# Optimization experiments

Measured on AMD Instinct MI355X. Metric: run time of the kernel, lower is better.

## Reference

```python
import jax, jax.numpy as jnp
import numpy as np

N = 32768      # total nodes per batched graph
E = 262144     # edges per batched graph (avg in-degree 8)
B = 64         # number of graphs in the batch (for mean_nodes readout)
DIN = 20
H = 512
BN_EPS = 1e-5


def setup_inputs() -> dict:
    key = jax.random.key(0)
    ks = jax.random.split(key, 24)
    p = lambda k, shape: jax.random.normal(k, shape, jnp.float32) * 0.02
    inp = {
        "x1": jax.random.normal(ks[0], (N, DIN), jnp.float32),
        "x2": jax.random.normal(ks[1], (N, DIN), jnp.float32),
        "src1": jax.random.randint(ks[2], (E,), 0, N, jnp.int32),
        "dst1": jax.random.randint(ks[3], (E,), 0, N, jnp.int32),
        "src2": jax.random.randint(ks[4], (E,), 0, N, jnp.int32),
        "dst2": jax.random.randint(ks[5], (E,), 0, N, jnp.int32),
        "gids1": jnp.repeat(jnp.arange(B, dtype=jnp.int32), N // B),
        "gids2": jnp.repeat(jnp.arange(B, dtype=jnp.int32), N // B),
        # shared parameters (applied to both graphs, as in the torch module)
        "W_init": p(ks[6], (DIN, H)), "b_init": jnp.zeros((H,), jnp.float32),
        "W1": p(ks[7], (H, H)), "b1": jnp.zeros((H,), jnp.float32),
        "W2": p(ks[8], (H, H)), "b2": jnp.zeros((H,), jnp.float32),
        "gamma1": jnp.ones((H,), jnp.float32), "beta1": jnp.zeros((H,), jnp.float32),
        "gamma2": jnp.ones((H,), jnp.float32), "beta2": jnp.zeros((H,), jnp.float32),
        "Wfc": p(ks[9], (2 * H, 256)), "bfc": jnp.zeros((256,), jnp.float32),
        "Wfc2": p(ks[10], (256, 1)), "bfc2": jnp.zeros((1,), jnp.float32),
    }
    return inp


def _bn_relu(z, gamma, beta):
    # BatchNorm1d in training mode: biased batch stats over the node axis
    mu = jnp.mean(z, axis=0)
    var = jnp.var(z, axis=0)
    return jax.nn.relu(gamma * (z - mu) * jax.lax.rsqrt(var + BN_EPS) + beta)


def _gin_mean(h, src, dst, W, b):
    # DGL GINConv(apply=Linear, aggregator='mean', eps=0):
    # out = Linear(h + mean_{j in N_in(v)} h_j); isolated nodes get 0 agg.
    msg_sum = jax.ops.segment_sum(h[src], dst, num_segments=N)      # [N,H]
    deg = jax.ops.segment_sum(jnp.ones((src.shape[0],), h.dtype), dst, num_segments=N)
    agg = msg_sum / jnp.maximum(deg, 1.0)[:, None]
    return (h + agg) @ W + b


def _encode(x, src, dst, gids, W_init, b_init, W1, b1, W2, b2,
            gamma1, beta1, gamma2, beta2):
    h0 = x @ W_init + b_init
    h1 = _bn_relu(_gin_mean(h0, src, dst, W1, b1), gamma1, beta1)
    h2 = _bn_relu(_gin_mean(h1, src, dst, W2, b2), gamma2, beta2)
    # dgl.mean_nodes: per-graph mean over nodes
    s = jax.ops.segment_sum(h2, gids, num_segments=B)               # [B,H]
    cnt = jax.ops.segment_sum(jnp.ones((h2.shape[0],), h2.dtype), gids, num_segments=B)
    return s / jnp.maximum(cnt, 1.0)[:, None]


def reference(x1, x2, src1, dst1, src2, dst2, gids1, gids2,
              W_init, b_init, W1, b1, W2, b2,
              gamma1, beta1, gamma2, beta2, Wfc, bfc, Wfc2, bfc2):
    g1_emb = _encode(x1, src1, dst1, gids1, W_init, b_init, W1, b1, W2, b2,
                     gamma1, beta1, gamma2, beta2)
    g2_emb = _encode(x2, src2, dst2, gids2, W_init, b_init, W1, b1, W2, b2,
                     gamma1, beta1, gamma2, beta2)
    x = jnp.concatenate([g1_emb, g2_emb], axis=1)                   # [B,2H]
    x = jax.nn.relu(x @ Wfc + bfc)
    return jax.nn.sigmoid(x @ Wfc2 + bfc2)                          # [B,1]
```

## Files before the change

kernel.cpp:

```cpp
#include <hip/hip_runtime.h>
#include <hip/hip_bf16.h>
#include <cstdint>

#define NN 32768
#define EE 262144
#define MM 65536
#define HH 512
#define BB 64
#define DIN 20
#define BN_EPS 1e-5f

__device__ __forceinline__ float bflo(uint32_t w) { return __builtin_bit_cast(float, w << 16); }
__device__ __forceinline__ float bfhi(uint32_t w) { return __builtin_bit_cast(float, w & 0xffff0000u); }
__device__ __forceinline__ uint32_t f2bf_u(float f) {
  uint32_t u = __builtin_bit_cast(uint32_t, f);
  return (u + 0x7fffu + ((u >> 16) & 1u)) >> 16;
}
__device__ __forceinline__ uint32_t pack2(float lo, float hi) {
  return f2bf_u(lo) | (f2bf_u(hi) << 16);
}

typedef float f32x4 __attribute__((ext_vector_type(4)));
typedef float f32x2 __attribute__((ext_vector_type(2)));

__device__ __forceinline__ void gl2lds16(const void* g, void* l) {
  __builtin_amdgcn_global_load_lds(
      (const __attribute__((address_space(1))) void*)g,
      (__attribute__((address_space(3))) void*)l, 16, 0, 0);
}

__global__ void prep_deg_kernel(const int* __restrict__ dst1, const int* __restrict__ dst2,
                                int* __restrict__ deg_cnt,
                                const float* __restrict__ W2, uint32_t* __restrict__ Wt8,
                                const float* __restrict__ Wi, const float* __restrict__ bi,
                                const float* __restrict__ W1, float* __restrict__ Wf) {
  int bid = blockIdx.x;
  if (bid < 2048) {
    int e = bid * 256 + threadIdx.x;
    int g = e >> 18, le = e & 0x3ffff;
    int d = (g ? dst2 : dst1)[le];
    atomicAdd(&deg_cnt[g * NN + d], 1);
  } else if (bid < 2304) {
    int idx = (bid - 2048) * 256 + threadIdx.x;
    int n = idx >> 7, k4 = idx & 127;
    int k = k4 * 4;
    float w0 = W2[(size_t)k * HH + n];
    float w1 = W2[(size_t)(k + 1) * HH + n];
    float w2v = W2[(size_t)(k + 2) * HH + n];
    float w3 = W2[(size_t)(k + 3) * HH + n];
    uint32_t p = __builtin_amdgcn_cvt_pk_fp8_f32(w0, w1, 0u, false);
    p = __builtin_amdgcn_cvt_pk_fp8_f32(w2v, w3, p, true);
    Wt8[(size_t)n * 128 + k4] = p;
  } else {
    int idx = (bid - 2304) * 256 + threadIdx.x;
    if (idx >= 21 * 512) return;
    int k = idx >> 9, n = idx & 511;
    float s = 0.f;
    if (k < 20) {
      const float* wr = Wi + (size_t)k * HH;
      for (int j = 0; j < HH; j++) s = fmaf(wr[j], W1[(size_t)j * HH + n], s);
    } else {
      for (int j = 0; j < HH; j++) s = fmaf(bi[j], W1[(size_t)j * HH + n], s);
    }
    Wf[idx] = s;
  }
}

__global__ void scan_kernel(const int* __restrict__ deg_cnt, int* __restrict__ offsets,
                            int* __restrict__ cursor) {
  int g = blockIdx.x;
  const int* d = deg_cnt + g * NN;
  int* off = offsets + g * (NN + 1);
  int* cur = cursor + g * NN;
  int t = threadIdx.x;
  int base = t * 32;
  int loc[32]; int s = 0;
#pragma unroll
  for (int i = 0; i < 32; i++) { loc[i] = d[base + i]; s += loc[i]; }
  __shared__ int sm[1024];
  sm[t] = s; __syncthreads();
  for (int ofs = 1; ofs < 1024; ofs <<= 1) {
    int v = sm[t];
    int add = (t >= ofs) ? sm[t - ofs] : 0;
    __syncthreads();
    sm[t] = v + add;
    __syncthreads();
  }
  int run = (t == 0) ? 0 : sm[t - 1];
#pragma unroll
  for (int i = 0; i < 32; i++) { off[base + i] = run; cur[base + i] = run; run += loc[i]; }
  if (t == 1023) off[NN] = run;
}

__global__ void scatter_kernel(const int* __restrict__ src1, const int* __restrict__ dst1,
                               const int* __restrict__ src2, const int* __restrict__ dst2,
                               int* __restrict__ cursor, int* __restrict__ csr) {
  int e = blockIdx.x * 256 + threadIdx.x;
  int g = e >> 18, le = e & 0x3ffff;
  int d = (g ? dst2 : dst1)[le];
  int s = (g ? src2 : src1)[le];
  int pos = atomicAdd(&cursor[g * NN + d], 1);
  csr[g * EE + pos] = s;
}

__global__ __launch_bounds__(512) void z1_kernel(const float* __restrict__ x1,
                          const float* __restrict__ x2,
                          const int* __restrict__ csr, const int* __restrict__ offsets,
                          const float* __restrict__ Wf, const float* __restrict__ b1,
                          uint32_t* __restrict__ z8, float* __restrict__ pstat) {
  __shared__ float xas[128][21];
  __shared__ float sred[512][8];
  int t = threadIdx.x;
  int r0 = blockIdx.x * 128;
  int g = r0 >> 15;
  const float* xg = g ? x2 : x1;
  const int* off = offsets + g * (NN + 1);
  const int* cs = csr + g * EE;

  {
    int row = t >> 2;
    int q = t & 3;
    int n = (r0 + row) & (NN - 1);
    int e0 = off[n], e1 = off[n + 1];
    float4 a4[5] = {};
    for (int e = e0 + q; e < e1; e += 4) {
      const float4* xr = (const float4*)(xg + (size_t)cs[e] * DIN);
#pragma unroll
      for (int k = 0; k < 5; k++) {
        float4 v = xr[k];
        a4[k].x += v.x; a4[k].y += v.y; a4[k].z += v.z; a4[k].w += v.w;
      }
    }
#pragma unroll
    for (int k = 0; k < 5; k++) {
      a4[k].x += __shfl_xor(a4[k].x, 1); a4[k].y += __shfl_xor(a4[k].y, 1);
      a4[k].z += __shfl_xor(a4[k].z, 1); a4[k].w += __shfl_xor(a4[k].w, 1);
      a4[k].x += __shfl_xor(a4[k].x, 2); a4[k].y += __shfl_xor(a4[k].y, 2);
      a4[k].z += __shfl_xor(a4[k].z, 2); a4[k].w += __shfl_xor(a4[k].w, 2);
    }
    if (q == 0) {
      float inv = (e1 > e0) ? 1.f / (float)(e1 - e0) : 0.f;
      const float4* xs = (const float4*)(xg + (size_t)n * DIN);
#pragma unroll
      for (int k = 0; k < 5; k++) {
        float4 v = xs[k];
        xas[row][k * 4 + 0] = fmaf(a4[k].x, inv, v.x);
        xas[row][k * 4 + 1] = fmaf(a4[k].y, inv, v.y);
        xas[row][k * 4 + 2] = fmaf(a4[k].z, inv, v.z);
        xas[row][k * 4 + 3] = fmaf(a4[k].w, inv, v.w);
      }
    }
  }
  __syncthreads();

  int col0 = (t & 127) * 4;
  int rq = t >> 7;

  float w[DIN][4];
#pragma unroll
  for (int k = 0; k < DIN; k++) {
    float4 wv = *(const float4*)(Wf + (size_t)k * HH + col0);
    w[k][0] = wv.x; w[k][1] = wv.y; w[k][2] = wv.z; w[k][3] = wv.w;
  }
  float4 bvv = *(const float4*)(Wf + (size_t)DIN * HH + col0);
  float4 b1v = *(const float4*)(b1 + col0);

  float s4[4] = {0.f, 0.f, 0.f, 0.f}, q4[4] = {0.f, 0.f, 0.f, 0.f};
  for (int rr = 0; rr < 32; rr++) {
    int row = rr * 4 + rq;
    int grow = r0 + row;
    int n = grow & (NN - 1);
    float bf = (off[n + 1] - off[n] > 0) ? 2.f : 1.f;
    float a0 = fmaf(bvv.x, bf, b1v.x), a1 = fmaf(bvv.y, bf, b1v.y);
    float a2 = fmaf(bvv.z, bf, b1v.z), a3 = fmaf(bvv.w, bf, b1v.w);
#pragma unroll
    for (int k = 0; k < DIN; k++) {
      float xv = xas[row][k];
      a0 = fmaf(xv, w[k][0], a0);
      a1 = fmaf(xv, w[k][1], a1);
      a2 = fmaf(xv, w[k][2], a2);
      a3 = fmaf(xv, w[k][3], a3);
    }
    s4[0] += a0; q4[0] = fmaf(a0, a0, q4[0]);
    s4[1] += a1; q4[1] = fmaf(a1, a1, q4[1]);
    s4[2] += a2; q4[2] = fmaf(a2, a2, q4[2]);
    s4[3] += a3; q4[3] = fmaf(a3, a3, q4[3]);
    uint32_t p8 = __builtin_amdgcn_cvt_pk_fp8_f32(a0, a1, 0u, false);
    p8 = __builtin_amdgcn_cvt_pk_fp8_f32(a2, a3, p8, true);
    z8[(size_t)grow * 128 + (col0 >> 2)] = p8;
  }

#pragma unroll
  for (int k = 0; k < 4; k++) { sred[t][k] = s4[k]; sred[t][4 + k] = q4[k]; }
  __syncthreads();
  if (t < 128) {
    float* p = pstat + (size_t)blockIdx.x * 1024 + (size_t)col0 * 2;
#pragma unroll
    for (int k = 0; k < 4; k++) {
      p[k * 2 + 0] = sred[t][k] + sred[t + 128][k] + sred[t + 256][k] + sred[t + 384][k];
      p[k * 2 + 1] = sred[t][4 + k] + sred[t + 128][4 + k] + sred[t + 256][4 + k] + sred[t + 384][4 + k];
    }
  }
}

__global__ void reduce_stats(const float* __restrict__ pstat, const float* __restrict__ gamma,
                             const float* __restrict__ beta, float* __restrict__ scsh) {
  int b = blockIdx.x;
  int g = b >> 4, cg = b & 15;
  int t = threadIdx.x;
  int c = cg * 32 + (t & 31);
  int s = t >> 5;
  const float2* p = (const float2*)pstat + ((size_t)(g * 256 + s * 32)) * 512 + c;
  float sum = 0.f, q = 0.f;
  for (int m = 0; m < 32; m++) { float2 v = p[(size_t)m * 512]; sum += v.x; q += v.y; }
  __shared__ float ls[8][64];
  ls[s][(t & 31) * 2] = sum; ls[s][(t & 31) * 2 + 1] = q;
  __syncthreads();
  if (t < 32) {
    float S = 0.f, Q = 0.f;
#pragma unroll
    for (int k = 0; k < 8; k++) { S += ls[k][t * 2]; Q += ls[k][t * 2 + 1]; }
    int cc = cg * 32 + t;
    float mu = S * (1.f / (float)NN);
    float var = fmaxf(Q * (1.f / (float)NN) - mu * mu, 0.f);
    float sc = gamma[cc] * rsqrtf(var + BN_EPS);
    scsh[g * 1024 + cc * 2] = sc;
    scsh[g * 1024 + cc * 2 + 1] = beta[cc] - mu * sc;
  }
}

__device__ __forceinline__ void bn_acc8_fp8(uint2 v, const float* sc, const float* sh, float* acc) {
  f32x2 f01 = __builtin_amdgcn_cvt_pk_f32_fp8(v.x, false);
  f32x2 f23 = __builtin_amdgcn_cvt_pk_f32_fp8(v.x, true);
  f32x2 f45 = __builtin_amdgcn_cvt_pk_f32_fp8(v.y, false);
  f32x2 f67 = __builtin_amdgcn_cvt_pk_f32_fp8(v.y, true);
  acc[0] += fmaxf(fmaf(f01.x, sc[0], sh[0]), 0.f);
  acc[1] += fmaxf(fmaf(f01.y, sc[1], sh[1]), 0.f);
  acc[2] += fmaxf(fmaf(f23.x, sc[2], sh[2]), 0.f);
  acc[3] += fmaxf(fmaf(f23.y, sc[3], sh[3]), 0.f);
  acc[4] += fmaxf(fmaf(f45.x, sc[4], sh[4]), 0.f);
  acc[5] += fmaxf(fmaf(f45.y, sc[5], sh[5]), 0.f);
  acc[6] += fmaxf(fmaf(f67.x, sc[6], sh[6]), 0.f);
  acc[7] += fmaxf(fmaf(f67.y, sc[7], sh[7]), 0.f);
}

__global__ __launch_bounds__(256) void aggbn_kernel(const uint32_t* __restrict__ z8,
                             uint32_t* __restrict__ u8,
                             const int* __restrict__ csr, const int* __restrict__ offsets,
                             const float* __restrict__ scsh) {
  int wid = (blockIdx.x * 256 + threadIdx.x) >> 6;
  int lane = threadIdx.x & 63;
  int g = wid >> 15, n = wid & (NN - 1);
  const int* off = offsets + g * (NN + 1);
  int e0 = off[n], e1 = off[n + 1];
  const int* cs = csr + g * EE;
  const uint32_t* base8 = z8 + (size_t)g * NN * 128 + lane * 2;

  uint2 hv8 = *(const uint2*)(base8 + (size_t)n * 128);

  const float4* ssp = (const float4*)(scsh + (size_t)g * HH * 2 + lane * 16);
  float4 ss0 = ssp[0], ss1 = ssp[1], ss2 = ssp[2], ss3 = ssp[3];
  float sc[8] = {ss0.x, ss0.z, ss1.x, ss1.z, ss2.x, ss2.z, ss3.x, ss3.z};
  float sh[8] = {ss0.y, ss0.w, ss1.y, ss1.w, ss2.y, ss2.w, ss3.y, ss3.w};
  float acc[8] = {0.f, 0.f, 0.f, 0.f, 0.f, 0.f, 0.f, 0.f};

  int e = e0;
  int rem = e1 - e0;
  int s0 = 0, s1 = 0, s2 = 0, s3 = 0;
  if (rem >= 4) { s0 = cs[e]; s1 = cs[e + 1]; s2 = cs[e + 2]; s3 = cs[e + 3]; }
  while (rem >= 4) {
    uint2 v0 = *(const uint2*)(base8 + (size_t)s0 * 128);
    uint2 v1 = *(const uint2*)(base8 + (size_t)s1 * 128);
    uint2 v2 = *(const uint2*)(base8 + (size_t)s2 * 128);
    uint2 v3 = *(const uint2*)(base8 + (size_t)s3 * 128);
    e += 4; rem -= 4;
    if (rem >= 4) { s0 = cs[e]; s1 = cs[e + 1]; s2 = cs[e + 2]; s3 = cs[e + 3]; }
    bn_acc8_fp8(v0, sc, sh, acc);
    bn_acc8_fp8(v1, sc, sh, acc);
    bn_acc8_fp8(v2, sc, sh, acc);
    bn_acc8_fp8(v3, sc, sh, acc);
  }
  for (; rem > 0; rem--, e++) {
    int s = cs[e];
    uint2 v = *(const uint2*)(base8 + (size_t)s * 128);
    bn_acc8_fp8(v, sc, sh, acc);
  }

  float inv = (e1 > e0) ? 1.f / (float)(e1 - e0) : 0.f;
  f32x2 h01 = __builtin_amdgcn_cvt_pk_f32_fp8(hv8.x, false);
  f32x2 h23 = __builtin_amdgcn_cvt_pk_f32_fp8(hv8.x, true);
  f32x2 h45 = __builtin_amdgcn_cvt_pk_f32_fp8(hv8.y, false);
  f32x2 h67 = __builtin_amdgcn_cvt_pk_f32_fp8(hv8.y, true);
  float hs[8] = {h01.x, h01.y, h23.x, h23.y, h45.x, h45.y, h67.x, h67.y};
  float o[8];
#pragma unroll
  for (int i = 0; i < 8; i++)
    o[i] = fmaxf(fmaf(hs[i], sc[i], sh[i]), 0.f) + acc[i] * inv;
  uint32_t q0 = __builtin_amdgcn_cvt_pk_fp8_f32(o[0], o[1], 0u, false);
  q0 = __builtin_amdgcn_cvt_pk_fp8_f32(o[2], o[3], q0, true);
  uint32_t q1 = __builtin_amdgcn_cvt_pk_fp8_f32(o[4], o[5], 0u, false);
  q1 = __builtin_amdgcn_cvt_pk_fp8_f32(o[6], o[7], q1, true);
  uint2 ov; ov.x = q0; ov.y = q1;
  *(uint2*)(u8 + (size_t)wid * 128 + lane * 2) = ov;
}

__global__ __launch_bounds__(256) void gemm_kernel(const uint8_t* __restrict__ A8,
                                                   const uint8_t* __restrict__ Bt8,
                                                   const float* __restrict__ bias,
                                                   uint16_t* __restrict__ C,
                                                   float* __restrict__ pstat) {
  __shared__ __align__(16) char lds[32768];
  uint8_t* sA = (uint8_t*)lds;
  uint8_t* sB = (uint8_t*)lds + 16384;
  const int tid = threadIdx.x;
  const int wave = tid >> 6;
  const int lane = tid & 63;
  const int bid = blockIdx.x;
  const int xcd = bid & 7;
  const int l = bid >> 3;
  const int nb = l & 3;
  const int mb = xcd * 64 + (l >> 2);
  const int m0 = mb * 128;
  const int n0 = nb * 128;
  const int fm = lane & 15;
  const int quad = lane >> 4;
  const int wr = wave >> 1, wc = wave & 1;

  const int sr = lane >> 3;
  const int slot = lane & 7;

  f32x4 acc[4][4] = {};
  for (int k0 = 0; k0 < HH; k0 += 128) {
    __syncthreads();
#pragma unroll
    for (int t = 0; t < 4; t++) {
      int R = t * 32 + wave * 8 + sr;
      int ksw = (slot ^ (R & 7)) * 16;
      gl2lds16(A8 + (size_t)(m0 + R) * HH + k0 + ksw, sA + R * 128 + slot * 16);
      gl2lds16(Bt8 + (size_t)(n0 + R) * HH + k0 + ksw, sB + R * 128 + slot * 16);
    }
    __syncthreads();
#pragma unroll
    for (int s2 = 0; s2 < 4; s2++) {
      const int k8 = s2 * 4 + quad;
      const int k16 = k8 >> 1;
      const int h8 = (k8 & 1) * 8;
      long a[4], b[4];
#pragma unroll
      for (int i = 0; i < 4; i++) {
        int r = wr * 64 + i * 16 + fm;
        a[i] = *(const long*)(sA + r * 128 + ((k16 ^ (r & 7)) * 16) + h8);
      }
#pragma unroll
      for (int j = 0; j < 4; j++) {
        int r = wc * 64 + j * 16 + fm;
        b[j] = *(const long*)(sB + r * 128 + ((k16 ^ (r & 7)) * 16) + h8);
      }
#pragma unroll
      for (int i = 0; i < 4; i++)
#pragma unroll
        for (int j = 0; j < 4; j++)
          acc[i][j] = __builtin_amdgcn_mfma_f32_16x16x32_fp8_fp8(a[i], b[j], acc[i][j], 0, 0, 0);
    }
  }

  float bj4[4];
#pragma unroll
  for (int j = 0; j < 4; j++) bj4[j] = bias[n0 + wc * 64 + j * 16 + fm];

  __syncthreads();
  float* ls = (float*)lds;
  if (tid < 256) ls[tid] = 0.f;
  __syncthreads();
#pragma unroll
  for (int j = 0; j < 4; j++) {
    int colloc = wc * 64 + j * 16 + fm;
    float sj = 0.f, qj = 0.f;
#pragma unroll
    for (int i = 0; i < 4; i++)
#pragma unroll
      for (int r = 0; r < 4; r++) {
        float f = acc[i][j][r] + bj4[j];
        sj += f; qj = fmaf(f, f, qj);
      }
    atomicAdd(&ls[colloc * 2], sj);
    atomicAdd(&ls[colloc * 2 + 1], qj);
  }
  __syncthreads();
  if (tid < 128) {
    float* p = pstat + (size_t)mb * 1024 + (size_t)(n0 + tid) * 2;
    p[0] = ls[tid * 2];
    p[1] = ls[tid * 2 + 1];
  }
  __syncthreads();

  uint16_t* sC = (uint16_t*)lds;
#pragma unroll
  for (int j = 0; j < 4; j++) {
    int col = wc * 64 + j * 16 + fm;
#pragma unroll
    for (int i = 0; i < 4; i++) {
      int rb = wr * 64 + i * 16 + quad * 4;
#pragma unroll
      for (int r = 0; r < 4; r++)
        sC[(rb + r) * 128 + col] = (uint16_t)f2bf_u(acc[i][j][r] + bj4[j]);
    }
  }
  __syncthreads();
  const int orow = tid >> 4;
  const int ocol = (tid & 15) * 8;
#pragma unroll
  for (int r8 = 0; r8 < 8; r8++) {
    int row = r8 * 16 + orow;
    uint4 v = *(const uint4*)(sC + row * 128 + ocol);
    *(uint4*)(C + (size_t)(m0 + row) * HH + n0 + ocol) = v;
  }
}

__global__ void bn2_readout(const uint16_t* __restrict__ z, const float* __restrict__ scsh,
                            const int* __restrict__ gids1, const int* __restrict__ gids2,
                            float* __restrict__ readout, float* __restrict__ cnt) {
  int blk = blockIdx.x;
  int r0 = blk * 128;
  int g = r0 >> 15;
  int lr = r0 & (NN - 1);
  int gid = (g ? gids2 : gids1)[lr];
  int t = threadIdx.x;
  int c = t * 2;
  const float* ss = scsh + (size_t)g * HH * 2;
  float sc0 = ss[c * 2], sh0 = ss[c * 2 + 1];
  float sc1 = ss[(c + 1) * 2], sh1 = ss[(c + 1) * 2 + 1];
  const uint32_t* p = (const uint32_t*)z + (size_t)r0 * 256 + t;
  float a0 = 0, a1 = 0;
  for (int r = 0; r < 128; r++) {
    uint32_t w = p[(size_t)r * 256];
    a0 += fmaxf(fmaf(bflo(w), sc0, sh0), 0.f);
    a1 += fmaxf(fmaf(bfhi(w), sc1, sh1), 0.f);
  }
  float* ro = readout + ((size_t)g * BB + gid) * HH;
  atomicAdd(&ro[c], a0);
  atomicAdd(&ro[c + 1], a1);
  if (t == 0) atomicAdd(&cnt[g * BB + gid], 128.f);
}

__global__ void final_kernel(const float* __restrict__ readout, const float* __restrict__ cnt,
                             const float* __restrict__ Wfc, const float* __restrict__ bfc,
                             const float* __restrict__ Wfc2, const float* __restrict__ bfc2,
                             float* __restrict__ out) {
  __shared__ float x[1024];
  __shared__ float red[256];
  int b = blockIdx.x, t = threadIdx.x;
  for (int i = t; i < 1024; i += 256) {
    int g = i >> 9, c = i & 511;
    float cc = cnt[g * BB + b];
    x[i] = readout[((size_t)g * BB + b) * HH + c] / fmaxf(cc, 1.f);
  }
  __syncthreads();
  float a0 = 0.f, a1 = 0.f, a2 = 0.f, a3 = 0.f;
  for (int i = 0; i < 1024; i += 4) {
    a0 = fmaf(x[i],     Wfc[(size_t)i * 256 + t],       a0);
    a1 = fmaf(x[i + 1], Wfc[(size_t)(i + 1) * 256 + t], a1);
    a2 = fmaf(x[i + 2], Wfc[(size_t)(i + 2) * 256 + t], a2);
    a3 = fmaf(x[i + 3], Wfc[(size_t)(i + 3) * 256 + t], a3);
  }
  float acc = bfc[t] + ((a0 + a1) + (a2 + a3));
  red[t] = fmaxf(acc, 0.f) * Wfc2[t];
  __syncthreads();
  for (int s = 128; s > 0; s >>= 1) {
    if (t < s) red[t] += red[t + s];
    __syncthreads();
  }
  if (t == 0) out[b] = 1.f / (1.f + expf(-(red[0] + bfc2[0])));
}

extern "C" void kernel_launch(void* const* d_in, const int* in_sizes, int n_in,
                              void* d_out, int out_size, void* d_ws, size_t ws_size,
                              hipStream_t stream) {
  const float* x1 = (const float*)d_in[0];
  const float* x2 = (const float*)d_in[1];
  const int* src1 = (const int*)d_in[2];
  const int* dst1 = (const int*)d_in[3];
  const int* src2 = (const int*)d_in[4];
  const int* dst2 = (const int*)d_in[5];
  const int* gids1 = (const int*)d_in[6];
  const int* gids2 = (const int*)d_in[7];
  const float* Wi = (const float*)d_in[8];
  const float* bi = (const float*)d_in[9];
  const float* W1 = (const float*)d_in[10];
  const float* b1 = (const float*)d_in[11];
  const float* W2 = (const float*)d_in[12];
  const float* b2 = (const float*)d_in[13];
  const float* gamma1 = (const float*)d_in[14];
  const float* beta1 = (const float*)d_in[15];
  const float* gamma2 = (const float*)d_in[16];
  const float* beta2 = (const float*)d_in[17];
  const float* Wfc = (const float*)d_in[18];
  const float* bfc = (const float*)d_in[19];
  const float* Wfc2 = (const float*)d_in[20];
  const float* bfc2 = (const float*)d_in[21];
  float* out = (float*)d_out;

  size_t off = 0;
  auto alloc = [&](size_t bytes) -> void* {
    void* p = (char*)d_ws + off;
    off += (bytes + 255) & ~(size_t)255;
    return p;
  };
  uint16_t* buf1 = (uint16_t*)alloc((size_t)MM * HH * 2);
  uint32_t* z8 = (uint32_t*)alloc((size_t)MM * HH);
  uint32_t* u8 = (uint32_t*)alloc((size_t)MM * HH);
  uint32_t* Wt8 = (uint32_t*)alloc((size_t)HH * HH);
  float* Wf = (float*)alloc((size_t)(DIN + 1) * HH * 4);
  int* csr = (int*)alloc((size_t)2 * EE * 4);
  int* offsets = (int*)alloc((size_t)2 * (NN + 1) * 4);
  int* cursor = (int*)alloc((size_t)2 * NN * 4);
  float* pbuf1 = (float*)alloc((size_t)512 * 512 * 2 * 4);
  float* pbuf2 = (float*)alloc((size_t)512 * 512 * 2 * 4);
  size_t zero_begin = off;
  int* deg_cnt = (int*)alloc((size_t)2 * NN * 4);
  float* readout = (float*)alloc((size_t)2 * BB * HH * 4);
  float* cnt = (float*)alloc((size_t)2 * BB * 4);
  size_t zero_end = off;
  float* scsh1 = (float*)alloc((size_t)2 * HH * 2 * 4);
  float* scsh2 = (float*)alloc((size_t)2 * HH * 2 * 4);
  (void)ws_size; (void)in_sizes; (void)n_in; (void)out_size;

  hipMemsetAsync((char*)d_ws + zero_begin, 0, zero_end - zero_begin, stream);

  prep_deg_kernel<<<2304 + 42, 256, 0, stream>>>(dst1, dst2, deg_cnt, W2, Wt8, Wi, bi, W1, Wf);
  scan_kernel<<<2, 1024, 0, stream>>>(deg_cnt, offsets, cursor);
  scatter_kernel<<<2048, 256, 0, stream>>>(src1, dst1, src2, dst2, cursor, csr);

  z1_kernel<<<MM / 128, 512, 0, stream>>>(x1, x2, csr, offsets, Wf, b1, z8, pbuf1);
  reduce_stats<<<32, 256, 0, stream>>>(pbuf1, gamma1, beta1, scsh1);

  aggbn_kernel<<<MM / 4, 256, 0, stream>>>(z8, u8, csr, offsets, scsh1);
  gemm_kernel<<<2048, 256, 0, stream>>>((const uint8_t*)u8, (const uint8_t*)Wt8, b2, buf1, pbuf2);
  reduce_stats<<<32, 256, 0, stream>>>(pbuf2, gamma2, beta2, scsh2);
  bn2_readout<<<MM / 128, 256, 0, stream>>>(buf1, scsh2, gids1, gids2, readout, cnt);

  final_kernel<<<BB, 256, 0, stream>>>(readout, cnt, Wfc, bfc, Wfc2, bfc2, out);
}
```

Measured before the change: 369.9 us.

## Enlarge GEMM tile to 256 rows, emit fp8 output, packed-f32 BN math

The second GEMM now uses 512-thread blocks with 256-row M tiles, so each B tile loaded into LDS is reused across twice as many rows and half as many per-block stat partials are written. Its epilogue writes fp8 instead of bf16, halving the intermediate written and then reread by the BN2 readout, which is rewritten to read fp8 with half the rows per thread and a shared-memory combine. The aggregation and readout BN math moves to packed f32x2 operations. Costs are more LDS per block, lower occupancy, and extra quantisation error from storing the pre-BN activations as fp8.

```diff
diff --git a/kernel.cpp b/kernel.cpp
--- a/kernel.cpp
+++ b/kernel.cpp
@@ -204,15 +204,16 @@
 }
 
 __global__ void reduce_stats(const float* __restrict__ pstat, const float* __restrict__ gamma,
-                             const float* __restrict__ beta, float* __restrict__ scsh) {
+                             const float* __restrict__ beta, float* __restrict__ scsh, int nsl) {
   int b = blockIdx.x;
   int g = b >> 4, cg = b & 15;
   int t = threadIdx.x;
   int c = cg * 32 + (t & 31);
   int s = t >> 5;
-  const float2* p = (const float2*)pstat + ((size_t)(g * 256 + s * 32)) * 512 + c;
+  int per = nsl >> 3;
+  const float2* p = (const float2*)pstat + ((size_t)(g * nsl + s * per)) * 512 + c;
   float sum = 0.f, q = 0.f;
-  for (int m = 0; m < 32; m++) { float2 v = p[(size_t)m * 512]; sum += v.x; q += v.y; }
+  for (int m = 0; m < per; m++) { float2 v = p[(size_t)m * 512]; sum += v.x; q += v.y; }
   __shared__ float ls[8][64];
   ls[s][(t & 31) * 2] = sum; ls[s][(t & 31) * 2 + 1] = q;
   __syncthreads();
@@ -229,19 +230,19 @@
   }
 }
 
-__device__ __forceinline__ void bn_acc8_fp8(uint2 v, const float* sc, const float* sh, float* acc) {
-  f32x2 f01 = __builtin_amdgcn_cvt_pk_f32_fp8(v.x, false);
-  f32x2 f23 = __builtin_amdgcn_cvt_pk_f32_fp8(v.x, true);
-  f32x2 f45 = __builtin_amdgcn_cvt_pk_f32_fp8(v.y, false);
-  f32x2 f67 = __builtin_amdgcn_cvt_pk_f32_fp8(v.y, true);
-  acc[0] += fmaxf(fmaf(f01.x, sc[0], sh[0]), 0.f);
-  acc[1] += fmaxf(fmaf(f01.y, sc[1], sh[1]), 0.f);
-  acc[2] += fmaxf(fmaf(f23.x, sc[2], sh[2]), 0.f);
-  acc[3] += fmaxf(fmaf(f23.y, sc[3], sh[3]), 0.f);
-  acc[4] += fmaxf(fmaf(f45.x, sc[4], sh[4]), 0.f);
-  acc[5] += fmaxf(fmaf(f45.y, sc[5], sh[5]), 0.f);
-  acc[6] += fmaxf(fmaf(f67.x, sc[6], sh[6]), 0.f);
-  acc[7] += fmaxf(fmaf(f67.y, sc[7], sh[7]), 0.f);
+__device__ __forceinline__ void bn_acc8_fp8(uint2 v, const f32x2* sc2, const f32x2* sh2,
+                                            f32x2* acc) {
+  f32x2 f[4];
+  f[0] = __builtin_amdgcn_cvt_pk_f32_fp8(v.x, false);
+  f[1] = __builtin_amdgcn_cvt_pk_f32_fp8(v.x, true);
+  f[2] = __builtin_amdgcn_cvt_pk_f32_fp8(v.y, false);
+  f[3] = __builtin_amdgcn_cvt_pk_f32_fp8(v.y, true);
+#pragma unroll
+  for (int i = 0; i < 4; i++) {
+    f32x2 y = f[i] * sc2[i] + sh2[i];
+    y.x = fmaxf(y.x, 0.f); y.y = fmaxf(y.y, 0.f);
+    acc[i] += y;
+  }
 }
 
 __global__ __launch_bounds__(256) void aggbn_kernel(const uint32_t* __restrict__ z8,
@@ -260,9 +261,12 @@
 
   const float4* ssp = (const float4*)(scsh + (size_t)g * HH * 2 + lane * 16);
   float4 ss0 = ssp[0], ss1 = ssp[1], ss2 = ssp[2], ss3 = ssp[3];
-  float sc[8] = {ss0.x, ss0.z, ss1.x, ss1.z, ss2.x, ss2.z, ss3.x, ss3.z};
-  float sh[8] = {ss0.y, ss0.w, ss1.y, ss1.w, ss2.y, ss2.w, ss3.y, ss3.w};
-  float acc[8] = {0.f, 0.f, 0.f, 0.f, 0.f, 0.f, 0.f, 0.f};
+  f32x2 sc2[4], sh2[4];
+  sc2[0] = f32x2{ss0.x, ss0.z}; sh2[0] = f32x2{ss0.y, ss0.w};
+  sc2[1] = f32x2{ss1.x, ss1.z}; sh2[1] = f32x2{ss1.y, ss1.w};
+  sc2[2] = f32x2{ss2.x, ss2.z}; sh2[2] = f32x2{ss2.y, ss2.w};
+  sc2[3] = f32x2{ss3.x, ss3.z}; sh2[3] = f32x2{ss3.y, ss3.w};
+  f32x2 acc2[4] = {f32x2{0.f, 0.f}, f32x2{0.f, 0.f}, f32x2{0.f, 0.f}, f32x2{0.f, 0.f}};
 
   int e = e0;
   int rem = e1 - e0;
@@ -275,15 +279,15 @@
     uint2 v3 = *(const uint2*)(base8 + (size_t)s3 * 128);
     e += 4; rem -= 4;
     if (rem >= 4) { s0 = cs[e]; s1 = cs[e + 1]; s2 = cs[e + 2]; s3 = cs[e + 3]; }
-    bn_acc8_fp8(v0, sc, sh, acc);
-    bn_acc8_fp8(v1, sc, sh, acc);
-    bn_acc8_fp8(v2, sc, sh, acc);
-    bn_acc8_fp8(v3, sc, sh, acc);
+    bn_acc8_fp8(v0, sc2, sh2, acc2);
+    bn_acc8_fp8(v1, sc2, sh2, acc2);
+    bn_acc8_fp8(v2, sc2, sh2, acc2);
+    bn_acc8_fp8(v3, sc2, sh2, acc2);
   }
   for (; rem > 0; rem--, e++) {
     int s = cs[e];
     uint2 v = *(const uint2*)(base8 + (size_t)s * 128);
-    bn_acc8_fp8(v, sc, sh, acc);
+    bn_acc8_fp8(v, sc2, sh2, acc2);
   }
 
   float inv = (e1 > e0) ? 1.f / (float)(e1 - e0) : 0.f;
@@ -291,11 +295,14 @@
   f32x2 h23 = __builtin_amdgcn_cvt_pk_f32_fp8(hv8.x, true);
   f32x2 h45 = __builtin_amdgcn_cvt_pk_f32_fp8(hv8.y, false);
   f32x2 h67 = __builtin_amdgcn_cvt_pk_f32_fp8(hv8.y, true);
-  float hs[8] = {h01.x, h01.y, h23.x, h23.y, h45.x, h45.y, h67.x, h67.y};
+  f32x2 hs[4] = {h01, h23, h45, h67};
   float o[8];
 #pragma unroll
-  for (int i = 0; i < 8; i++)
-    o[i] = fmaxf(fmaf(hs[i], sc[i], sh[i]), 0.f) + acc[i] * inv;
+  for (int i = 0; i < 4; i++) {
+    f32x2 y = hs[i] * sc2[i] + sh2[i];
+    o[2 * i]     = fmaxf(y.x, 0.f) + acc2[i].x * inv;
+    o[2 * i + 1] = fmaxf(y.y, 0.f) + acc2[i].y * inv;
+  }
   uint32_t q0 = __builtin_amdgcn_cvt_pk_fp8_f32(o[0], o[1], 0u, false);
   q0 = __builtin_amdgcn_cvt_pk_fp8_f32(o[2], o[3], q0, true);
   uint32_t q1 = __builtin_amdgcn_cvt_pk_fp8_f32(o[4], o[5], 0u, false);
@@ -304,14 +311,14 @@
   *(uint2*)(u8 + (size_t)wid * 128 + lane * 2) = ov;
 }
 
-__global__ __launch_bounds__(256) void gemm_kernel(const uint8_t* __restrict__ A8,
+__global__ __launch_bounds__(512) void gemm_kernel(const uint8_t* __restrict__ A8,
                                                    const uint8_t* __restrict__ Bt8,
                                                    const float* __restrict__ bias,
-                                                   uint16_t* __restrict__ C,
+                                                   uint8_t* __restrict__ Z2,
                                                    float* __restrict__ pstat) {
-  __shared__ __align__(16) char lds[32768];
+  __shared__ __align__(16) char lds[49152];
   uint8_t* sA = (uint8_t*)lds;
-  uint8_t* sB = (uint8_t*)lds + 16384;
+  uint8_t* sB = (uint8_t*)lds + 32768;
   const int tid = threadIdx.x;
   const int wave = tid >> 6;
   const int lane = tid & 63;
@@ -319,8 +326,8 @@
   const int xcd = bid & 7;
   const int l = bid >> 3;
   const int nb = l & 3;
-  const int mb = xcd * 64 + (l >> 2);
-  const int m0 = mb * 128;
+  const int mb = xcd * 32 + (l >> 2);
+  const int m0 = mb * 256;
   const int n0 = nb * 128;
   const int fm = lane & 15;
   const int quad = lane >> 4;
@@ -334,10 +341,11 @@
     __syncthreads();
 #pragma unroll
     for (int t = 0; t < 4; t++) {
-      int R = t * 32 + wave * 8 + sr;
+      int R = t * 64 + wave * 8 + sr;
       int ksw = (slot ^ (R & 7)) * 16;
       gl2lds16(A8 + (size_t)(m0 + R) * HH + k0 + ksw, sA + R * 128 + slot * 16);
-      gl2lds16(Bt8 + (size_t)(n0 + R) * HH + k0 + ksw, sB + R * 128 + slot * 16);
+      if (t < 2)
+        gl2lds16(Bt8 + (size_t)(n0 + R) * HH + k0 + ksw, sB + R * 128 + slot * 16);
     }
     __syncthreads();
 #pragma unroll
@@ -396,28 +404,45 @@
 
   uint16_t* sC = (uint16_t*)lds;
 #pragma unroll
-  for (int j = 0; j < 4; j++) {
-    int col = wc * 64 + j * 16 + fm;
-#pragma unroll
-    for (int i = 0; i < 4; i++) {
-      int rb = wr * 64 + i * 16 + quad * 4;
-#pragma unroll
-      for (int r = 0; r < 4; r++)
-        sC[(rb + r) * 128 + col] = (uint16_t)f2bf_u(acc[i][j][r] + bj4[j]);
-    }
-  }
-  __syncthreads();
-  const int orow = tid >> 4;
-  const int ocol = (tid & 15) * 8;
-#pragma unroll
-  for (int r8 = 0; r8 < 8; r8++) {
-    int row = r8 * 16 + orow;
-    uint4 v = *(const uint4*)(sC + row * 128 + ocol);
-    *(uint4*)(C + (size_t)(m0 + row) * HH + n0 + ocol) = v;
-  }
-}
-
-__global__ void bn2_readout(const uint16_t* __restrict__ z, const float* __restrict__ scsh,
+  for (int h = 0; h < 2; h++) {
+    if ((wr >> 1) == h) {
+      int lrb = (wr & 1) * 64;
+#pragma unroll
+      for (int j = 0; j < 4; j++) {
+        int col = wc * 64 + j * 16 + fm;
+#pragma unroll
+        for (int i = 0; i < 4; i++) {
+          int rb = lrb + i * 16 + quad * 4;
+#pragma unroll
+          for (int r = 0; r < 4; r++)
+            sC[(rb + r) * 136 + col] = (uint16_t)f2bf_u(acc[i][j][r] + bj4[j]);
+        }
+      }
+    }
+    __syncthreads();
+    int orow = tid >> 3;
+    int oc16 = (tid & 7) * 16;
+#pragma unroll
+    for (int r2 = 0; r2 < 2; r2++) {
+      int row = r2 * 64 + orow;
+      uint4 va = *(const uint4*)(sC + row * 136 + oc16);
+      uint4 vb = *(const uint4*)(sC + row * 136 + oc16 + 8);
+      uint32_t wv[8] = {va.x, va.y, va.z, va.w, vb.x, vb.y, vb.z, vb.w};
+      uint4 o8;
+      uint32_t* op = (uint32_t*)&o8;
+#pragma unroll
+      for (int q = 0; q < 4; q++) {
+        uint32_t p8 = __builtin_amdgcn_cvt_pk_fp8_f32(bflo(wv[2 * q]), bfhi(wv[2 * q]), 0u, false);
+        p8 = __builtin_amdgcn_cvt_pk_fp8_f32(bflo(wv[2 * q + 1]), bfhi(wv[2 * q + 1]), p8, true);
+        op[q] = p8;
+      }
+      *(uint4*)(Z2 + (size_t)(m0 + h * 128 + row) * HH + n0 + oc16) = o8;
+    }
+    __syncthreads();
+  }
+}
+
+__global__ void bn2_readout(const uint32_t* __restrict__ z2, const float* __restrict__ scsh,
                             const int* __restrict__ gids1, const int* __restrict__ gids2,
                             float* __restrict__ readout, float* __restrict__ cnt) {
   int blk = blockIdx.x;
@@ -426,20 +451,33 @@
   int lr = r0 & (NN - 1);
   int gid = (g ? gids2 : gids1)[lr];
   int t = threadIdx.x;
-  int c = t * 2;
-  const float* ss = scsh + (size_t)g * HH * 2;
-  float sc0 = ss[c * 2], sh0 = ss[c * 2 + 1];
-  float sc1 = ss[(c + 1) * 2], sh1 = ss[(c + 1) * 2 + 1];
-  const uint32_t* p = (const uint32_t*)z + (size_t)r0 * 256 + t;
-  float a0 = 0, a1 = 0;
-  for (int r = 0; r < 128; r++) {
-    uint32_t w = p[(size_t)r * 256];
-    a0 += fmaxf(fmaf(bflo(w), sc0, sh0), 0.f);
-    a1 += fmaxf(fmaf(bfhi(w), sc1, sh1), 0.f);
-  }
-  float* ro = readout + ((size_t)g * BB + gid) * HH;
-  atomicAdd(&ro[c], a0);
-  atomicAdd(&ro[c + 1], a1);
+  int cg = t & 127, rh = t >> 7;
+  const float* ss = scsh + (size_t)g * HH * 2 + cg * 8;
+  float4 s0 = *(const float4*)ss, s1 = *(const float4*)(ss + 4);
+  f32x2 sc01 = f32x2{s0.x, s0.z}, sh01 = f32x2{s0.y, s0.w};
+  f32x2 sc23 = f32x2{s1.x, s1.z}, sh23 = f32x2{s1.y, s1.w};
+  const uint32_t* p = z2 + (size_t)(r0 + rh * 64) * 128 + cg;
+  f32x2 a01 = f32x2{0.f, 0.f}, a23 = f32x2{0.f, 0.f};
+  for (int r = 0; r < 64; r++) {
+    uint32_t w = p[(size_t)r * 128];
+    f32x2 f01 = __builtin_amdgcn_cvt_pk_f32_fp8(w, false);
+    f32x2 f23 = __builtin_amdgcn_cvt_pk_f32_fp8(w, true);
+    f32x2 y0 = f01 * sc01 + sh01;
+    f32x2 y1 = f23 * sc23 + sh23;
+    y0.x = fmaxf(y0.x, 0.f); y0.y = fmaxf(y0.y, 0.f);
+    y1.x = fmaxf(y1.x, 0.f); y1.y = fmaxf(y1.y, 0.f);
+    a01 += y0; a23 += y1;
+  }
+  __shared__ float sr2[128][4];
+  if (rh) { sr2[cg][0] = a01.x; sr2[cg][1] = a01.y; sr2[cg][2] = a23.x; sr2[cg][3] = a23.y; }
+  __syncthreads();
+  if (!rh) {
+    float* ro = readout + ((size_t)g * BB + gid) * HH;
+    atomicAdd(&ro[cg * 4 + 0], a01.x + sr2[cg][0]);
+    atomicAdd(&ro[cg * 4 + 1], a01.y + sr2[cg][1]);
+    atomicAdd(&ro[cg * 4 + 2], a23.x + sr2[cg][2]);
+    atomicAdd(&ro[cg * 4 + 3], a23.y + sr2[cg][3]);
+  }
   if (t == 0) atomicAdd(&cnt[g * BB + gid], 128.f);
 }
 
@@ -506,16 +544,16 @@
     off += (bytes + 255) & ~(size_t)255;
     return p;
   };
-  uint16_t* buf1 = (uint16_t*)alloc((size_t)MM * HH * 2);
   uint32_t* z8 = (uint32_t*)alloc((size_t)MM * HH);
   uint32_t* u8 = (uint32_t*)alloc((size_t)MM * HH);
+  uint8_t* z2o = (uint8_t*)alloc((size_t)MM * HH);
   uint32_t* Wt8 = (uint32_t*)alloc((size_t)HH * HH);
   float* Wf = (float*)alloc((size_t)(DIN + 1) * HH * 4);
   int* csr = (int*)alloc((size_t)2 * EE * 4);
   int* offsets = (int*)alloc((size_t)2 * (NN + 1) * 4);
   int* cursor = (int*)alloc((size_t)2 * NN * 4);
   float* pbuf1 = (float*)alloc((size_t)512 * 512 * 2 * 4);
-  float* pbuf2 = (float*)alloc((size_t)512 * 512 * 2 * 4);
+  float* pbuf2 = (float*)alloc((size_t)256 * 512 * 2 * 4);
   size_t zero_begin = off;
   int* deg_cnt = (int*)alloc((size_t)2 * NN * 4);
   float* readout = (float*)alloc((size_t)2 * BB * HH * 4);
@@ -532,12 +570,12 @@
   scatter_kernel<<<2048, 256, 0, stream>>>(src1, dst1, src2, dst2, cursor, csr);
 
   z1_kernel<<<MM / 128, 512, 0, stream>>>(x1, x2, csr, offsets, Wf, b1, z8, pbuf1);
-  reduce_stats<<<32, 256, 0, stream>>>(pbuf1, gamma1, beta1, scsh1);
+  reduce_stats<<<32, 256, 0, stream>>>(pbuf1, gamma1, beta1, scsh1, 256);
 
   aggbn_kernel<<<MM / 4, 256, 0, stream>>>(z8, u8, csr, offsets, scsh1);
-  gemm_kernel<<<2048, 256, 0, stream>>>((const uint8_t*)u8, (const uint8_t*)Wt8, b2, buf1, pbuf2);
-  reduce_stats<<<32, 256, 0, stream>>>(pbuf2, gamma2, beta2, scsh2);
-  bn2_readout<<<MM / 128, 256, 0, stream>>>(buf1, scsh2, gids1, gids2, readout, cnt);
+  gemm_kernel<<<1024, 512, 0, stream>>>((const uint8_t*)u8, (const uint8_t*)Wt8, b2, z2o, pbuf2);
+  reduce_stats<<<32, 256, 0, stream>>>(pbuf2, gamma2, beta2, scsh2, 128);
+  bn2_readout<<<512, 256, 0, stream>>>((const uint32_t*)z2o, scsh2, gids1, gids2, readout, cnt);
 
   final_kernel<<<BB, 256, 0, stream>>>(readout, cnt, Wfc, bfc, Wfc2, bfc2, out);
 }
```

New measurement: 381.9 us. +3.2%, slower.
